# Kernel tuning notes

Measured on AMD Instinct MI355X. Metric: run time of the kernel, lower is better.

## Reference

```python
import jax, jax.numpy as jnp
import numpy as np
import math

B, C_IN, H, W = 1, 3, 96, 96
FEAT_C, GDIM, BLOCK = 64, 8, 16
TW, TH = (W + BLOCK - 1) // BLOCK, (H + BLOCK - 1) // BLOCK
TWO_PI = 2.0 * math.pi
EPS = 1e-6


def setup_inputs() -> dict:
    key = jax.random.key(0)
    ks = jax.random.split(key, 3)
    inp = jax.random.normal(ks[0], (B, C_IN, H, W), jnp.float32)
    w_enc = jax.random.normal(ks[1], (FEAT_C, C_IN, 3, 3), jnp.float32) / np.sqrt(C_IN * 9).astype(np.float32)
    b_enc = jnp.zeros((FEAT_C,), jnp.float32)
    w_head = jax.random.normal(ks[2], (GDIM, FEAT_C), jnp.float32) / np.sqrt(FEAT_C).astype(np.float32)
    b_head = jnp.zeros((GDIM,), jnp.float32)
    return {"inp": inp, "w_enc": w_enc, "b_enc": b_enc, "w_head": w_head, "b_head": b_head}


def _rasterize_one(rgb, scale, theta, x_ndc, y_ndc):
    # rgb (N,3), scale (N,2), theta (N,), x_ndc/y_ndc (N,) ; N = H*W gaussians
    c, s = jnp.cos(theta), jnp.sin(theta)
    v0, v1 = scale[:, 0] ** 2, scale[:, 1] ** 2
    # Sigma = R diag(s)^2 R^T
    S00 = c * c * v0 + s * s * v1
    S01 = c * s * (v0 - v1)
    S11 = s * s * v0 + c * c * v1
    det = S00 * S11 - S01 * S01
    inv_det = 1.0 / det
    ca, cb, cc = S11 * inv_det, -S01 * inv_det, S00 * inv_det  # conic (a,b,c)
    bmid = 0.5 * (S00 + S11)
    lam1 = bmid + jnp.sqrt(jnp.maximum(0.1, bmid * bmid - det))
    radius = jax.lax.stop_gradient(jnp.ceil(3.0 * jnp.sqrt(lam1)))
    # ndc -> pixel centers
    cx = 0.5 * W * (x_ndc + 1.0) - 0.5
    cy = 0.5 * H * (y_ndc + 1.0) - 0.5
    cxs, cys = jax.lax.stop_gradient(cx), jax.lax.stop_gradient(cy)
    # tile bbox (C-style trunc-toward-zero casts, matching the CUDA kernel)
    tmin_x = jnp.clip(((cxs - radius) / BLOCK).astype(jnp.int32), 0, TW)
    tmax_x = jnp.clip(((cxs + radius) / BLOCK).astype(jnp.int32) + 1, 0, TW)
    tmin_y = jnp.clip(((cys - radius) / BLOCK).astype(jnp.int32), 0, TH)
    tmax_y = jnp.clip(((cys + radius) / BLOCK).astype(jnp.int32) + 1, 0, TH)
    # pixel grid, row-major (i over H, j over W); P = H*W
    prow, pcol = jnp.meshgrid(jnp.arange(H), jnp.arange(W), indexing='ij')
    px = pcol.reshape(-1).astype(jnp.float32)
    py = prow.reshape(-1).astype(jnp.float32)
    tx = (pcol.reshape(-1) // BLOCK).astype(jnp.int32)
    ty = (prow.reshape(-1) // BLOCK).astype(jnp.int32)
    dx = cx[:, None] - px[None, :]  # (N,P)
    dy = cy[:, None] - py[None, :]
    sigma = 0.5 * (ca[:, None] * dx * dx + cc[:, None] * dy * dy) + cb[:, None] * dx * dy
    alpha = jnp.minimum(0.999, jnp.exp(-sigma))  # opacity == 1
    valid = ((sigma >= 0.0) & (alpha >= 1.0 / 255.0)
             & (radius[:, None] > 0)
             & (tx[None, :] >= tmin_x[:, None]) & (tx[None, :] < tmax_x[:, None])
             & (ty[None, :] >= tmin_y[:, None]) & (ty[None, :] < tmax_y[:, None]))
    wgt = jnp.where(valid, alpha, 0.0)
    out = jnp.einsum('np,nc->pc', wgt, rgb)  # order-independent sum compositing
    return out.reshape(H, W, 3).transpose(2, 0, 1)  # (3,H,W)


def _forward(inp, w_enc, b_enc, w_head, b_head):
    Bn = inp.shape[0]
    feat = jax.lax.conv_general_dilated(
        inp, w_enc, (1, 1), 'SAME',
        dimension_numbers=('NCHW', 'OIHW', 'NCHW')) + b_enc[None, :, None, None]
    pred = jnp.einsum('bchw,oc->bhwo', feat, w_head) + b_head  # 1x1 head
    pred = pred.reshape(Bn, H * W, GDIM)
    rgb = pred[..., 0:3]
    theta = jax.nn.sigmoid(pred[..., 3]) * TWO_PI
    scale = jax.nn.sigmoid(pred[..., 4:6]) * 0.5 + EPS
    offset = jnp.tanh(pred[..., 6:8])
    # get_coord(h_inp, w_inp): coord[...,0] varies over width, coord[...,1] over height
    xg = (2.0 * jnp.arange(H, dtype=jnp.float32) / H - 1.0)[:, None]
    yg = (2.0 * jnp.arange(W, dtype=jnp.float32) / W - 1.0)[None, :]
    coord0 = jnp.broadcast_to(yg, (H, W)).reshape(-1)
    coord1 = jnp.broadcast_to(xg, (H, W)).reshape(-1)
    x_ndc = coord0[None, :] + 2.0 * offset[..., 0] / W - 1.0 / W
    y_ndc = coord1[None, :] + 2.0 * offset[..., 1] / H - 1.0 / H
    img = jax.vmap(_rasterize_one)(rgb, scale, theta, x_ndc, y_ndc)
    return jnp.clip(img, 0.0, 1.0)  # (B,3,H,W)


def reference(inp, w_enc, b_enc, w_head, b_head):
    return _forward(inp, w_enc, b_enc, w_head, b_head)
```

## Files before the change

### kernel.cpp

```cpp
#include <hip/hip_runtime.h>
#include <math.h>

#define HH   96
#define WW   96
#define NPIX 9216
#define TWT  6
#define THT  6

__device__ __forceinline__ float fast_sigmoid(float x) {
    return 1.0f / (1.0f + __expf(-x));
}
__device__ __forceinline__ float fast_tanh(float x) {
    return 1.0f - 2.0f / (__expf(2.0f * x) + 1.0f);
}


__global__ __launch_bounds__(256) void gauss_params_kernel(
    const float* __restrict__ inp, const float* __restrict__ w_enc,
    const float* __restrict__ b_enc, const float* __restrict__ w_head,
    const float* __restrict__ b_head,
    float4* __restrict__ gpA, float4* __restrict__ gpB, int* __restrict__ gb)
{
    __shared__ float wcomb[8][27];
    __shared__ float bcomb[8];
    const int tid = threadIdx.x;

    if (tid < 216) {
        const int o = tid / 27, r = tid % 27;
        float acc = 0.0f;
        for (int c = 0; c < 64; ++c)
            acc = fmaf(w_head[o * 64 + c], w_enc[c * 27 + r], acc);
        wcomb[o][r] = acc;
    } else if (tid < 224) {
        const int o = tid - 216;
        float acc = b_head[o];
        for (int c = 0; c < 64; ++c)
            acc = fmaf(w_head[o * 64 + c], b_enc[c], acc);
        bcomb[o] = acc;
    }
    __syncthreads();

    const int p   = blockIdx.x * 256 + tid;
    const int row = p / WW, col = p % WW;

    float patch[27];
    #pragma unroll
    for (int i = 0; i < 3; ++i) {
        #pragma unroll
        for (int dy = 0; dy < 3; ++dy) {
            const int y = row + dy - 1;
            #pragma unroll
            for (int dx = 0; dx < 3; ++dx) {
                const int x = col + dx - 1;
                float v = 0.0f;
                if (y >= 0 && y < HH && x >= 0 && x < WW)
                    v = inp[i * NPIX + y * WW + x];
                patch[(i * 3 + dy) * 3 + dx] = v;
            }
        }
    }

    float pred[8];
    #pragma unroll
    for (int o = 0; o < 8; ++o) {
        float acc = bcomb[o];
        #pragma unroll
        for (int r = 0; r < 27; ++r)
            acc = fmaf(wcomb[o][r], patch[r], acc);
        pred[o] = acc;
    }

    const float theta = fast_sigmoid(pred[3]) * 6.28318530717958647692f;
    const float cth = __cosf(theta), sth = __sinf(theta);
    const float s0 = fast_sigmoid(pred[4]) * 0.5f + 1e-6f;
    const float s1 = fast_sigmoid(pred[5]) * 0.5f + 1e-6f;
    const float v0 = s0 * s0, v1 = s1 * s1;
    const float S00 = cth * cth * v0 + sth * sth * v1;
    const float S01 = cth * sth * (v0 - v1);
    const float S11 = sth * sth * v0 + cth * cth * v1;
    const float det = S00 * S11 - S01 * S01;
    const float inv_det = 1.0f / det;
    const float ca = S11 * inv_det;
    const float cb = -S01 * inv_det;
    const float cc = S00 * inv_det;
    const float bmid = 0.5f * (S00 + S11);
    const float lam1 = bmid + sqrtf(fmaxf(0.1f, bmid * bmid - det));
    const float radius = ceilf(3.0f * sqrtf(lam1));
    const float off0 = fast_tanh(pred[6]);
    const float off1 = fast_tanh(pred[7]);
    const float coord0 = 2.0f * (float)col / (float)WW - 1.0f;
    const float coord1 = 2.0f * (float)row / (float)HH - 1.0f;
    const float x_ndc = coord0 + 2.0f * off0 / (float)WW - 1.0f / (float)WW;
    const float y_ndc = coord1 + 2.0f * off1 / (float)HH - 1.0f / (float)HH;
    const float cx = 0.5f * (float)WW * (x_ndc + 1.0f) - 0.5f;
    const float cy = 0.5f * (float)HH * (y_ndc + 1.0f) - 0.5f;

    int tminx = (int)((cx - radius) / 16.0f);
    int tmaxx = (int)((cx + radius) / 16.0f) + 1;
    int tminy = (int)((cy - radius) / 16.0f);
    int tmaxy = (int)((cy + radius) / 16.0f) + 1;
    tminx = min(max(tminx, 0), TWT); tmaxx = min(max(tmaxx, 0), TWT);
    tminy = min(max(tminy, 0), THT); tmaxy = min(max(tmaxy, 0), THT);
    if (!(radius > 0.0f)) { tmaxx = tminx; tmaxy = tminy; }

    gpA[p] = make_float4(cx, cy, ca, cb);
    gpB[p] = make_float4(cc, pred[0], pred[1], pred[2]);
    gb[p]  = tminx | (tmaxx << 8) | (tminy << 16) | (tmaxy << 24);
}

__global__ __launch_bounds__(256) void rasterize_kernel(
    const float4* __restrict__ gpA, const float4* __restrict__ gpB,
    const int* __restrict__ gb, float* __restrict__ out)
{
    const int t     = blockIdx.x * 256 + threadIdx.x;
    const int p     = t >> 3;
    const int slice = t & 7;
    const int row = p / WW, col = p % WW;
    const int tx = col >> 4, ty = row >> 4;
    const float px = (float)col, py = (float)row;

    float aR = 0.0f, aG = 0.0f, aB = 0.0f;
    for (int idx = slice; idx < 81; idx += 8) {
        const int wr = idx / 9, wc = idx - wr * 9;
        const int gr = row - 3 + wr;
        const int gc = col - 3 + wc;
        if (gr < 0 || gr >= HH || gc < 0 || gc >= WW) continue;
        const int n = gr * WW + gc;
        const float4 A  = gpA[n];
        const float4 Bv = gpB[n];
        const float dx = A.x - px;
        const float dy = A.y - py;
        const float sigma = 0.5f * (A.z * dx * dx + Bv.x * dy * dy) + A.w * dx * dy;
        const float alpha = fminf(0.999f, __expf(-sigma));
        const int bnd = gb[n];
        const bool valid = (sigma >= 0.0f) && (alpha >= (1.0f / 255.0f)) &&
                           (tx >= (bnd & 0xff)) && (tx < ((bnd >> 8) & 0xff)) &&
                           (ty >= ((bnd >> 16) & 0xff)) && (ty < ((bnd >> 24) & 0xff));
        if (valid) {
            aR = fmaf(alpha, Bv.y, aR);
            aG = fmaf(alpha, Bv.z, aG);
            aB = fmaf(alpha, Bv.w, aB);
        }
    }

    aR += __shfl_xor(aR, 1); aR += __shfl_xor(aR, 2); aR += __shfl_xor(aR, 4);
    aG += __shfl_xor(aG, 1); aG += __shfl_xor(aG, 2); aG += __shfl_xor(aG, 4);
    aB += __shfl_xor(aB, 1); aB += __shfl_xor(aB, 2); aB += __shfl_xor(aB, 4);

    if (slice < 3) {
        const float v = (slice == 0) ? aR : (slice == 1) ? aG : aB;
        out[slice * NPIX + p] = fminf(fmaxf(v, 0.0f), 1.0f);
    }
}

extern "C" void kernel_launch(void* const* d_in, const int* in_sizes, int n_in,
                              void* d_out, int out_size, void* d_ws, size_t ws_size,
                              hipStream_t stream)
{
    const float* inp    = (const float*)d_in[0];
    const float* w_enc  = (const float*)d_in[1];
    const float* b_enc  = (const float*)d_in[2];
    const float* w_head = (const float*)d_in[3];
    const float* b_head = (const float*)d_in[4];
    float* out = (float*)d_out;

    float4* gpA = (float4*)d_ws;
    float4* gpB = gpA + NPIX;
    int*    gb  = (int*)(gpB + NPIX);

    gauss_params_kernel<<<36, 256, 0, stream>>>(inp, w_enc, b_enc, w_head, b_head, gpA, gpB, gb);
    rasterize_kernel<<<(NPIX * 8) / 256, 256, 0, stream>>>(gpA, gpB, gb, out);
}
```

Baseline: 72.23 us.

## Fuse gaussian parameter and rasterize kernels with per-tile shared-memory halo

New measurement: 79.25 us. 9.7% more time.

```diff
diff --git a/kernel.cpp b/kernel.cpp
--- a/kernel.cpp
+++ b/kernel.cpp
@@ -6,6 +6,8 @@
 #define NPIX 9216
 #define TWT  6
 #define THT  6
+#define SW   24
+#define NSRC (SW*SW)
 
 __device__ __forceinline__ float fast_sigmoid(float x) {
     return 1.0f / (1.0f + __expf(-x));
@@ -14,16 +16,21 @@
     return 1.0f - 2.0f / (__expf(2.0f * x) + 1.0f);
 }
 
-
-__global__ __launch_bounds__(256) void gauss_params_kernel(
+__global__ __launch_bounds__(256) void gauss_fused_kernel(
     const float* __restrict__ inp, const float* __restrict__ w_enc,
     const float* __restrict__ b_enc, const float* __restrict__ w_head,
-    const float* __restrict__ b_head,
-    float4* __restrict__ gpA, float4* __restrict__ gpB, int* __restrict__ gb)
+    const float* __restrict__ b_head, float* __restrict__ out)
 {
-    __shared__ float wcomb[8][27];
-    __shared__ float bcomb[8];
+    __shared__ float  wcomb[8][27];
+    __shared__ float  bcomb[8];
+    __shared__ float4 lgA[NSRC];
+    __shared__ float4 lgB[NSRC];
+    __shared__ int    lgb[NSRC];
+
     const int tid = threadIdx.x;
+    const int bx = blockIdx.x % 6, by = blockIdx.x / 6;
+    const int r0 = by * 16, c0 = bx * 16;
+    const int sr0 = r0 - 3, sc0 = c0 - 3;
 
     if (tid < 216) {
         const int o = tid / 27, r = tid % 27;
@@ -40,117 +47,108 @@
     }
     __syncthreads();
 
-    const int p   = blockIdx.x * 256 + tid;
-    const int row = p / WW, col = p % WW;
+    for (int s = tid; s < NSRC; s += 256) {
+        const int sr = s / SW, sc = s - sr * SW;
+        const int gr = sr0 + sr, gc = sc0 + sc;
+        if (gr < 0 || gr >= HH || gc < 0 || gc >= WW) continue;
 
-    float patch[27];
-    #pragma unroll
-    for (int i = 0; i < 3; ++i) {
+        float pred[8];
         #pragma unroll
-        for (int dy = 0; dy < 3; ++dy) {
-            const int y = row + dy - 1;
+        for (int o = 0; o < 8; ++o) pred[o] = bcomb[o];
+        #pragma unroll
+        for (int i = 0; i < 3; ++i) {
             #pragma unroll
-            for (int dx = 0; dx < 3; ++dx) {
-                const int x = col + dx - 1;
-                float v = 0.0f;
-                if (y >= 0 && y < HH && x >= 0 && x < WW)
-                    v = inp[i * NPIX + y * WW + x];
-                patch[(i * 3 + dy) * 3 + dx] = v;
+            for (int dy = 0; dy < 3; ++dy) {
+                const int y = gr + dy - 1;
+                #pragma unroll
+                for (int dx = 0; dx < 3; ++dx) {
+                    const int x = gc + dx - 1;
+                    float v = 0.0f;
+                    if (y >= 0 && y < HH && x >= 0 && x < WW)
+                        v = inp[i * NPIX + y * WW + x];
+                    const int r = (i * 3 + dy) * 3 + dx;
+                    #pragma unroll
+                    for (int o = 0; o < 8; ++o)
+                        pred[o] = fmaf(wcomb[o][r], v, pred[o]);
+                }
             }
         }
+
+        const float theta = fast_sigmoid(pred[3]) * 6.28318530717958647692f;
+        const float cth = __cosf(theta), sth = __sinf(theta);
+        const float s0 = fast_sigmoid(pred[4]) * 0.5f + 1e-6f;
+        const float s1 = fast_sigmoid(pred[5]) * 0.5f + 1e-6f;
+        const float v0 = s0 * s0, v1 = s1 * s1;
+        const float S00 = cth * cth * v0 + sth * sth * v1;
+        const float S01 = cth * sth * (v0 - v1);
+        const float S11 = sth * sth * v0 + cth * cth * v1;
+        const float det = S00 * S11 - S01 * S01;
+        const float inv_det = 1.0f / det;
+        const float ca = S11 * inv_det;
+        const float cb = -S01 * inv_det;
+        const float cc = S00 * inv_det;
+        const float bmid = 0.5f * (S00 + S11);
+        const float lam1 = bmid + sqrtf(fmaxf(0.1f, bmid * bmid - det));
+        const float radius = ceilf(3.0f * sqrtf(lam1));
+        const float off0 = fast_tanh(pred[6]);
+        const float off1 = fast_tanh(pred[7]);
+        const float coord0 = 2.0f * (float)gc / (float)WW - 1.0f;
+        const float coord1 = 2.0f * (float)gr / (float)HH - 1.0f;
+        const float x_ndc = coord0 + 2.0f * off0 / (float)WW - 1.0f / (float)WW;
+        const float y_ndc = coord1 + 2.0f * off1 / (float)HH - 1.0f / (float)HH;
+        const float cx = 0.5f * (float)WW * (x_ndc + 1.0f) - 0.5f;
+        const float cy = 0.5f * (float)HH * (y_ndc + 1.0f) - 0.5f;
+
+        int tminx = (int)((cx - radius) / 16.0f);
+        int tmaxx = (int)((cx + radius) / 16.0f) + 1;
+        int tminy = (int)((cy - radius) / 16.0f);
+        int tmaxy = (int)((cy + radius) / 16.0f) + 1;
+        tminx = min(max(tminx, 0), TWT); tmaxx = min(max(tmaxx, 0), TWT);
+        tminy = min(max(tminy, 0), THT); tmaxy = min(max(tmaxy, 0), THT);
+        if (!(radius > 0.0f)) { tmaxx = tminx; tmaxy = tminy; }
+
+        lgA[s] = make_float4(cx, cy, ca, cb);
+        lgB[s] = make_float4(cc, pred[0], pred[1], pred[2]);
+        lgb[s] = tminx | (tmaxx << 8) | (tminy << 16) | (tmaxy << 24);
     }
+    __syncthreads();
 
-    float pred[8];
-    #pragma unroll
-    for (int o = 0; o < 8; ++o) {
-        float acc = bcomb[o];
-        #pragma unroll
-        for (int r = 0; r < 27; ++r)
-            acc = fmaf(wcomb[o][r], patch[r], acc);
-        pred[o] = acc;
-    }
-
-    const float theta = fast_sigmoid(pred[3]) * 6.28318530717958647692f;
-    const float cth = __cosf(theta), sth = __sinf(theta);
-    const float s0 = fast_sigmoid(pred[4]) * 0.5f + 1e-6f;
-    const float s1 = fast_sigmoid(pred[5]) * 0.5f + 1e-6f;
-    const float v0 = s0 * s0, v1 = s1 * s1;
-    const float S00 = cth * cth * v0 + sth * sth * v1;
-    const float S01 = cth * sth * (v0 - v1);
-    const float S11 = sth * sth * v0 + cth * cth * v1;
-    const float det = S00 * S11 - S01 * S01;
-    const float inv_det = 1.0f / det;
-    const float ca = S11 * inv_det;
-    const float cb = -S01 * inv_det;
-    const float cc = S00 * inv_det;
-    const float bmid = 0.5f * (S00 + S11);
-    const float lam1 = bmid + sqrtf(fmaxf(0.1f, bmid * bmid - det));
-    const float radius = ceilf(3.0f * sqrtf(lam1));
-    const float off0 = fast_tanh(pred[6]);
-    const float off1 = fast_tanh(pred[7]);
-    const float coord0 = 2.0f * (float)col / (float)WW - 1.0f;
-    const float coord1 = 2.0f * (float)row / (float)HH - 1.0f;
-    const float x_ndc = coord0 + 2.0f * off0 / (float)WW - 1.0f / (float)WW;
-    const float y_ndc = coord1 + 2.0f * off1 / (float)HH - 1.0f / (float)HH;
-    const float cx = 0.5f * (float)WW * (x_ndc + 1.0f) - 0.5f;
-    const float cy = 0.5f * (float)HH * (y_ndc + 1.0f) - 0.5f;
-
-    int tminx = (int)((cx - radius) / 16.0f);
-    int tmaxx = (int)((cx + radius) / 16.0f) + 1;
-    int tminy = (int)((cy - radius) / 16.0f);
-    int tmaxy = (int)((cy + radius) / 16.0f) + 1;
-    tminx = min(max(tminx, 0), TWT); tmaxx = min(max(tmaxx, 0), TWT);
-    tminy = min(max(tminy, 0), THT); tmaxy = min(max(tmaxy, 0), THT);
-    if (!(radius > 0.0f)) { tmaxx = tminx; tmaxy = tminy; }
-
-    gpA[p] = make_float4(cx, cy, ca, cb);
-    gpB[p] = make_float4(cc, pred[0], pred[1], pred[2]);
-    gb[p]  = tminx | (tmaxx << 8) | (tminy << 16) | (tmaxy << 24);
-}
-
-__global__ __launch_bounds__(256) void rasterize_kernel(
-    const float4* __restrict__ gpA, const float4* __restrict__ gpB,
-    const int* __restrict__ gb, float* __restrict__ out)
-{
-    const int t     = blockIdx.x * 256 + threadIdx.x;
-    const int p     = t >> 3;
-    const int slice = t & 7;
-    const int row = p / WW, col = p % WW;
+    const int lr = tid >> 4, lc = tid & 15;
+    const int row = r0 + lr, col = c0 + lc;
     const int tx = col >> 4, ty = row >> 4;
     const float px = (float)col, py = (float)row;
 
     float aR = 0.0f, aG = 0.0f, aB = 0.0f;
-    for (int idx = slice; idx < 81; idx += 8) {
-        const int wr = idx / 9, wc = idx - wr * 9;
+    #pragma unroll
+    for (int wr = 0; wr < 9; ++wr) {
         const int gr = row - 3 + wr;
-        const int gc = col - 3 + wc;
-        if (gr < 0 || gr >= HH || gc < 0 || gc >= WW) continue;
-        const int n = gr * WW + gc;
-        const float4 A  = gpA[n];
-        const float4 Bv = gpB[n];
-        const float dx = A.x - px;
-        const float dy = A.y - py;
-        const float sigma = 0.5f * (A.z * dx * dx + Bv.x * dy * dy) + A.w * dx * dy;
-        const float alpha = fminf(0.999f, __expf(-sigma));
-        const int bnd = gb[n];
-        const bool valid = (sigma >= 0.0f) && (alpha >= (1.0f / 255.0f)) &&
-                           (tx >= (bnd & 0xff)) && (tx < ((bnd >> 8) & 0xff)) &&
-                           (ty >= ((bnd >> 16) & 0xff)) && (ty < ((bnd >> 24) & 0xff));
-        if (valid) {
-            aR = fmaf(alpha, Bv.y, aR);
-            aG = fmaf(alpha, Bv.z, aG);
-            aB = fmaf(alpha, Bv.w, aB);
+        if (gr < 0 || gr >= HH) continue;
+        const int sbase = (lr + wr) * SW + lc;
+        for (int wc = 0; wc < 9; ++wc) {
+            const int gc = col - 3 + wc;
+            if (gc < 0 || gc >= WW) continue;
+            const int s = sbase + wc;
+            const float4 A  = lgA[s];
+            const float4 Bv = lgB[s];
+            const float dx = A.x - px;
+            const float dy = A.y - py;
+            const float sigma = 0.5f * (A.z * dx * dx + Bv.x * dy * dy) + A.w * dx * dy;
+            const float alpha = fminf(0.999f, __expf(-sigma));
+            const int bnd = lgb[s];
+            const bool valid = (sigma >= 0.0f) && (alpha >= (1.0f / 255.0f)) &&
+                               (tx >= (bnd & 0xff)) && (tx < ((bnd >> 8) & 0xff)) &&
+                               (ty >= ((bnd >> 16) & 0xff)) && (ty < ((bnd >> 24) & 0xff));
+            if (valid) {
+                aR = fmaf(alpha, Bv.y, aR);
+                aG = fmaf(alpha, Bv.z, aG);
+                aB = fmaf(alpha, Bv.w, aB);
+            }
         }
     }
-
-    aR += __shfl_xor(aR, 1); aR += __shfl_xor(aR, 2); aR += __shfl_xor(aR, 4);
-    aG += __shfl_xor(aG, 1); aG += __shfl_xor(aG, 2); aG += __shfl_xor(aG, 4);
-    aB += __shfl_xor(aB, 1); aB += __shfl_xor(aB, 2); aB += __shfl_xor(aB, 4);
-
-    if (slice < 3) {
-        const float v = (slice == 0) ? aR : (slice == 1) ? aG : aB;
-        out[slice * NPIX + p] = fminf(fmaxf(v, 0.0f), 1.0f);
-    }
+    const int p = row * WW + col;
+    out[0 * NPIX + p] = fminf(fmaxf(aR, 0.0f), 1.0f);
+    out[1 * NPIX + p] = fminf(fmaxf(aG, 0.0f), 1.0f);
+    out[2 * NPIX + p] = fminf(fmaxf(aB, 0.0f), 1.0f);
 }
 
 extern "C" void kernel_launch(void* const* d_in, const int* in_sizes, int n_in,
@@ -164,10 +162,5 @@
     const float* b_head = (const float*)d_in[4];
     float* out = (float*)d_out;
 
-    float4* gpA = (float4*)d_ws;
-    float4* gpB = gpA + NPIX;
-    int*    gb  = (int*)(gpB + NPIX);
-
-    gauss_params_kernel<<<36, 256, 0, stream>>>(inp, w_enc, b_enc, w_head, b_head, gpA, gpB, gb);
-    rasterize_kernel<<<(NPIX * 8) / 256, 256, 0, stream>>>(gpA, gpB, gb, out);
+    gauss_fused_kernel<<<36, 256, 0, stream>>>(inp, w_enc, b_enc, w_head, b_head, out);
 }
```
